# Kernel optimization log

Hardware: AMD Instinct MI355X
Metric: run time of the kernel (lower is better)

The kernel has to match this reference:

```python
import jax, jax.numpy as jnp
import numpy as np

DIM = 192
HEADS = 4
EPS = 1e-12  # matches torch F.normalize eps


def setup_inputs() -> dict:
    key = jax.random.key(0)
    ks = jax.random.split(key, 5)
    x = jax.random.normal(ks[0], (8, DIM, 128, 128), dtype=jnp.float32)
    # 1x1 conv_in: (3*dim, dim)
    w_in = jax.random.normal(ks[1], (3 * DIM, DIM), dtype=jnp.float32) * (1.0 / np.sqrt(DIM))
    # depthwise 3x3: OIHW with I=1, groups=3*dim -> (3*dim, 1, 3, 3)
    w_dw = jax.random.normal(ks[2], (3 * DIM, 1, 3, 3), dtype=jnp.float32) * (1.0 / 3.0)
    temperature = jnp.ones((HEADS, 1, 1), dtype=jnp.float32)
    # 1x1 conv_out: (dim, dim)
    w_out = jax.random.normal(ks[3], (DIM, DIM), dtype=jnp.float32) * (1.0 / np.sqrt(DIM))
    return {"x": x, "w_in": w_in, "w_dw": w_dw, "temperature": temperature, "w_out": w_out}


def _l2norm(t):
    n = jnp.sqrt(jnp.sum(t * t, axis=-1, keepdims=True))
    return t / jnp.maximum(n, EPS)


def reference(x, w_in, w_dw, temperature, w_out):
    b, c, h, w = x.shape
    # 1x1 pointwise conv (no bias)
    qkv = jnp.einsum('oc,bchw->bohw', w_in, x)
    # 3x3 depthwise conv, padding=1
    qkv = jax.lax.conv_general_dilated(
        qkv, w_dw, window_strides=(1, 1), padding=((1, 1), (1, 1)),
        feature_group_count=3 * c,
        dimension_numbers=('NCHW', 'OIHW', 'NCHW'))
    q, k, v = jnp.split(qkv, 3, axis=1)
    cph = c // HEADS  # channels per head
    hw = h * w
    q = q.reshape(b, HEADS, cph, hw)
    k = k.reshape(b, HEADS, cph, hw)
    v = v.reshape(b, HEADS, cph, hw)
    q = _l2norm(q)
    k = _l2norm(k)
    # channel-wise attention: [b, head, cph, cph]
    attn = jnp.einsum('bhcn,bhdn->bhcd', q, k) * temperature
    attn = jax.nn.softmax(attn, axis=-1)
    out = jnp.einsum('bhcd,bhdn->bhcn', attn, v)
    out = out.reshape(b, c, h, w)
    out = jnp.einsum('oc,bchw->bohw', w_out, out)
    return out
```

## Files before the change

### kernel.cpp

```cpp
#include <hip/hip_runtime.h>
#include <hip/hip_bf16.h>

#define HW 16384
#define NB 8
#define NC 192
#define NC3 576
#define NHEADS 4
#define CPH 48

typedef __attribute__((ext_vector_type(8))) short short8v;
typedef __attribute__((ext_vector_type(4))) float f32x4;

__device__ __forceinline__ float bf2f(ushort u) {
    union { unsigned int u; float f; } w; w.u = ((unsigned int)u) << 16; return w.f;
}
__device__ __forceinline__ ushort f2bf(float f) {
    union { float f; unsigned int u; } w; w.f = f;
    return (ushort)((w.u + 0x7FFFu + ((w.u >> 16) & 1u)) >> 16);
}

__global__ __launch_bounds__(256) void k_prep(const float* __restrict__ w_in,
                                              ushort* __restrict__ w_bf) {
    int i = blockIdx.x * 256 + threadIdx.x;
    if (i < NC3 * NC) w_bf[i] = f2bf(w_in[i]);
}

template<bool B_F32, bool OUT_F32>
__global__ __launch_bounds__(256) void k_gemm2(
    const ushort* __restrict__ Abase, long aStride, int MT,
    const void* __restrict__ Bp, long bStride,
    void* __restrict__ Op, long oStride)
{
    __shared__ ushort Bs[64 * 200];
    const int t = threadIdx.x;
    const int nt = blockIdx.x, b = blockIdx.y;

    {
        const int n0 = (t & 15) * 4;
        const int k0 = (t >> 4) * 12;
        ushort vals[12][4];
        if constexpr (B_F32) {
            const float* B = (const float*)Bp + (long)b * bStride
                           + (long)k0 * HW + nt * 64 + n0;
            #pragma unroll
            for (int kk = 0; kk < 12; kk++) {
                float4 v = *(const float4*)(B + (long)kk * HW);
                vals[kk][0] = f2bf(v.x); vals[kk][1] = f2bf(v.y);
                vals[kk][2] = f2bf(v.z); vals[kk][3] = f2bf(v.w);
            }
        } else {
            const ushort* B = (const ushort*)Bp + (long)b * bStride
                            + (long)k0 * HW + nt * 64 + n0;
            #pragma unroll
            for (int kk = 0; kk < 12; kk++) {
                ushort4 v = *(const ushort4*)(B + (long)kk * HW);
                vals[kk][0] = v.x; vals[kk][1] = v.y;
                vals[kk][2] = v.z; vals[kk][3] = v.w;
            }
        }
        #pragma unroll
        for (int i = 0; i < 4; i++) {
            #pragma unroll
            for (int seg = 0; seg < 3; seg++) {
                ushort4 w4;
                w4.x = vals[seg * 4 + 0][i];
                w4.y = vals[seg * 4 + 1][i];
                w4.z = vals[seg * 4 + 2][i];
                w4.w = vals[seg * 4 + 3][i];
                *(ushort4*)&Bs[(n0 + i) * 200 + k0 + seg * 4] = w4;
            }
        }
    }
    __syncthreads();

    const int wid = t >> 6, lane = t & 63;
    const int wm = (wid >> 1) * 32, wn = (wid & 1) * 32;
    const int lr = lane & 15, lk = lane >> 4;
    const ushort* Ab = Abase + (long)b * aStride;
    const ushort* Bs0 = &Bs[(wn + lr) * 200 + lk * 8];
    const f32x4 z4 = {0.f, 0.f, 0.f, 0.f};

    for (int ot = 0; ot < MT; ot++) {
        f32x4 acc[2][2];
        acc[0][0] = z4; acc[0][1] = z4; acc[1][0] = z4; acc[1][1] = z4;
        const ushort* Ar0 = Ab + (long)(ot * 64 + wm + lr) * NC + lk * 8;
        const ushort* Ar1 = Ar0 + 16 * NC;
        #pragma unroll
        for (int ks = 0; ks < 6; ks++) {
            short8v a0 = *(const short8v*)(Ar0 + ks * 32);
            short8v a1 = *(const short8v*)(Ar1 + ks * 32);
            short8v b0 = *(const short8v*)(Bs0 + ks * 32);
            short8v b1 = *(const short8v*)(Bs0 + 16 * 200 + ks * 32);
            acc[0][0] = __builtin_amdgcn_mfma_f32_16x16x32_bf16(a0, b0, acc[0][0], 0, 0, 0);
            acc[0][1] = __builtin_amdgcn_mfma_f32_16x16x32_bf16(a0, b1, acc[0][1], 0, 0, 0);
            acc[1][0] = __builtin_amdgcn_mfma_f32_16x16x32_bf16(a1, b0, acc[1][0], 0, 0, 0);
            acc[1][1] = __builtin_amdgcn_mfma_f32_16x16x32_bf16(a1, b1, acc[1][1], 0, 0, 0);
        }
        #pragma unroll
        for (int mi = 0; mi < 2; mi++) {
            #pragma unroll
            for (int ni = 0; ni < 2; ni++) {
                long gm = (long)ot * 64 + wm + mi * 16 + lk * 4;
                long gn = (long)nt * 64 + wn + ni * 16 + lr;
                if constexpr (OUT_F32) {
                    float* O = (float*)Op + (long)b * oStride + gm * HW + gn;
                    #pragma unroll
                    for (int r = 0; r < 4; r++) O[(long)r * HW] = acc[mi][ni][r];
                } else {
                    ushort* O = (ushort*)Op + (long)b * oStride + gm * HW + gn;
                    #pragma unroll
                    for (int r = 0; r < 4; r++) O[(long)r * HW] = f2bf(acc[mi][ni][r]);
                }
            }
        }
    }
}

__global__ __launch_bounds__(256) void k_dwconv(
    const ushort* __restrict__ qkv, const float* __restrict__ w_dw,
    ushort* __restrict__ qkv_dw, float* __restrict__ sumsq)
{
    __shared__ ushort tile[130 * 144];
    __shared__ float red[4];
    const int t = threadIdx.x;
    const int c = blockIdx.x, b = blockIdx.y;

    if (t < 144) { tile[t] = 0; tile[129 * 144 + t] = 0; }
    if (t < 128) { tile[(t + 1) * 144 + 7] = 0; tile[(t + 1) * 144 + 136] = 0; }

    const ushort* src = qkv + ((long)b * NC3 + c) * HW;
    #pragma unroll
    for (int i = 0; i < 8; i++) {
        int idx = t + 256 * i;
        int row = idx >> 4;
        int col8 = idx & 15;
        *(short8v*)(tile + (row + 1) * 144 + 8 + col8 * 8) =
            *(const short8v*)(src + (long)idx * 8);
    }
    __syncthreads();

    float wv[9];
    #pragma unroll
    for (int j = 0; j < 9; j++) wv[j] = w_dw[c * 9 + j];

    const int cb = (t & 15) * 8;
    const int r0 = (t >> 4) * 8;
    float win[3][16];

    auto load_row = [&](int tr, int slot) {
        #pragma unroll
        for (int j = 0; j < 4; j++) {
            ushort4 v = *(const ushort4*)(tile + tr * 144 + 4 + cb + j * 4);
            win[slot][j * 4 + 0] = bf2f(v.x);
            win[slot][j * 4 + 1] = bf2f(v.y);
            win[slot][j * 4 + 2] = bf2f(v.z);
            win[slot][j * 4 + 3] = bf2f(v.w);
        }
    };

    load_row(r0, 0);
    load_row(r0 + 1, 1);
    float ssq = 0.f;
    ushort* dst = qkv_dw + ((long)b * NC3 + c) * HW + (long)r0 * 128 + cb;

    #pragma unroll
    for (int rr = 0; rr < 8; rr++) {
        load_row(r0 + rr + 2, (rr + 2) % 3);
        const int s0 = rr % 3, s1 = (rr + 1) % 3, s2 = (rr + 2) % 3;
        short8v o;
        #pragma unroll
        for (int oc = 0; oc < 8; oc++) {
            float a = win[s0][oc + 3] * wv[0] + win[s0][oc + 4] * wv[1] + win[s0][oc + 5] * wv[2]
                    + win[s1][oc + 3] * wv[3] + win[s1][oc + 4] * wv[4] + win[s1][oc + 5] * wv[5]
                    + win[s2][oc + 3] * wv[6] + win[s2][oc + 4] * wv[7] + win[s2][oc + 5] * wv[8];
            ssq += a * a;
            o[oc] = (short)f2bf(a);
        }
        *(short8v*)(dst + rr * 128) = o;
    }

    #pragma unroll
    for (int off = 32; off > 0; off >>= 1) ssq += __shfl_down(ssq, off, 64);
    if ((t & 63) == 0) red[t >> 6] = ssq;
    __syncthreads();
    if (t == 0 && c < 2 * NC) sumsq[b * (2 * NC) + c] = red[0] + red[1] + red[2] + red[3];
}

__global__ __launch_bounds__(256) void k_scores(
    const ushort* __restrict__ qkv_dw, float* __restrict__ Spart)
{
    const int bh = blockIdx.x, ks = blockIdx.y;
    const int b = bh >> 2, h = bh & 3;
    const int t = threadIdx.x, wid = t >> 6, lane = t & 63;
    const int lr = lane & 15, lk = lane >> 4;
    const ushort* qb = qkv_dw + ((long)b * NC3 + h * CPH) * HW;
    const ushort* kb = qb + (long)NC * HW;

    const f32x4 z4 = {0.f, 0.f, 0.f, 0.f};
    f32x4 acc[3][3];
    #pragma unroll
    for (int i = 0; i < 3; i++) {
        #pragma unroll
        for (int j = 0; j < 3; j++) acc[i][j] = z4;
    }

    const int kstart = ks * 2048 + wid * 512;
    for (int k0 = kstart; k0 < kstart + 512; k0 += 32) {
        short8v a[3], bv[3];
        #pragma unroll
        for (int i = 0; i < 3; i++) {
            a[i]  = *(const short8v*)(qb + (long)(i * 16 + lr) * HW + k0 + lk * 8);
            bv[i] = *(const short8v*)(kb + (long)(i * 16 + lr) * HW + k0 + lk * 8);
        }
        #pragma unroll
        for (int mi = 0; mi < 3; mi++) {
            #pragma unroll
            for (int ni = 0; ni < 3; ni++)
                acc[mi][ni] = __builtin_amdgcn_mfma_f32_16x16x32_bf16(a[mi], bv[ni], acc[mi][ni], 0, 0, 0);
        }
    }

    __shared__ float Sb[4 * 48 * 48];
    #pragma unroll
    for (int mi = 0; mi < 3; mi++) {
        #pragma unroll
        for (int ni = 0; ni < 3; ni++) {
            #pragma unroll
            for (int r = 0; r < 4; r++)
                Sb[wid * 2304 + (mi * 16 + lk * 4 + r) * 48 + ni * 16 + lr] = acc[mi][ni][r];
        }
    }
    __syncthreads();
    float* outp = Spart + ((long)ks * 32 + bh) * 2304;
    for (int i = t; i < 2304; i += 256)
        outp[i] = Sb[i] + Sb[2304 + i] + Sb[4608 + i] + Sb[6912 + i];
}

__global__ __launch_bounds__(256) void k_final(
    const float* __restrict__ Spart, const float* __restrict__ sumsq,
    const float* __restrict__ temperature, const float* __restrict__ wout,
    ushort* __restrict__ Mmat)
{
    const int bh = blockIdx.x, b = bh >> 2, h = bh & 3;
    const int t = threadIdx.x;
    __shared__ float S[48 * 48];
    __shared__ float P[48 * 48];
    __shared__ float invq[48], invk[48];
    if (t < 48) {
        invq[t] = 1.f / fmaxf(sqrtf(sumsq[b * (2 * NC) + h * CPH + t]), 1e-12f);
        invk[t] = 1.f / fmaxf(sqrtf(sumsq[b * (2 * NC) + NC + h * CPH + t]), 1e-12f);
    }
    __syncthreads();
    const float T = temperature[h];
    for (int i = t; i < 2304; i += 256) {
        float s = 0.f;
        #pragma unroll
        for (int p = 0; p < 8; p++) s += Spart[((long)p * 32 + bh) * 2304 + i];
        int cc = i / 48, dd = i - cc * 48;
        S[i] = s * invq[cc] * invk[dd] * T;
    }
    __syncthreads();
    if (t < 48) {
        float m = -1e30f;
        for (int d = 0; d < 48; d++) m = fmaxf(m, S[t * 48 + d]);
        float sum = 0.f;
        for (int d = 0; d < 48; d++) { float e = __expf(S[t * 48 + d] - m); P[t * 48 + d] = e; sum += e; }
        float inv = 1.f / sum;
        for (int d = 0; d < 48; d++) P[t * 48 + d] *= inv;
    }
    __syncthreads();
    for (int i = t; i < NC * CPH; i += 256) {
        int o = i / 48, d = i - (i / 48) * 48;
        float a = 0.f;
        for (int c2 = 0; c2 < 48; c2++)
            a += wout[o * NC + h * CPH + c2] * P[c2 * 48 + d];
        Mmat[(long)b * NC * NC + (long)o * NC + h * CPH + d] = f2bf(a);
    }
}

extern "C" void kernel_launch(void* const* d_in, const int* in_sizes, int n_in,
                              void* d_out, int out_size, void* d_ws, size_t ws_size,
                              hipStream_t stream)
{
    (void)in_sizes; (void)n_in; (void)out_size;
    const float* x     = (const float*)d_in[0];
    const float* w_in  = (const float*)d_in[1];
    const float* w_dw  = (const float*)d_in[2];
    const float* temp  = (const float*)d_in[3];
    const float* w_out = (const float*)d_in[4];
    float* outp = (float*)d_out;

    const long QKV_BYTES = (long)NB * NC3 * HW * 2;
    char* ws = (char*)d_ws;
    if (ws_size < 305172480UL) return;
    ushort* qkv    = (ushort*)(ws);
    ushort* qkv_dw = (ushort*)(ws + QKV_BYTES);
    ushort* w_bf   = (ushort*)(ws + 2 * QKV_BYTES);
    float*  sumsq  = (float*) (ws + 302211072L);
    float*  Spart  = (float*) (ws + 302223360L);
    ushort* Mmat   = (ushort*)(ws + 304582656L);

    k_prep<<<dim3(432), 256, 0, stream>>>(w_in, w_bf);

    k_gemm2<true, false><<<dim3(256, NB), 256, 0, stream>>>(
        w_bf, 0L, 9, x, (long)NC * HW, qkv, (long)NC3 * HW);

    k_dwconv<<<dim3(NC3, NB), 256, 0, stream>>>(qkv, w_dw, qkv_dw, sumsq);

    k_scores<<<dim3(32, 8), 256, 0, stream>>>(qkv_dw, Spart);

    k_final<<<dim3(32), 256, 0, stream>>>(Spart, sumsq, temp, w_out, Mmat);

    k_gemm2<false, true><<<dim3(256, NB), 256, 0, stream>>>(
        Mmat, (long)NC * NC, 3, qkv_dw + (long)(2 * NC) * HW, (long)NC3 * HW,
        outp, (long)NC * HW);
}
```

Baseline: 301.1 us.

## Restructure pointwise GEMMs: register-resident A tile, pipelined B staging, vectorized stores

The 1x1-conv GEMM kernel changes its decomposition. Each block now keeps one 64-row weight tile in registers and walks over several 64-column spatial chunks, loading the next B chunk from global memory while the current one is converted and computed. The MFMA operands are swapped so each lane holds four consecutive spatial outputs, which allows float4/ushort4 stores in place of strided scalar ones. The LDS row pitch also changes from 200 to 208. The trade-off is that each block re-reads the x/v columns once per output-row tile instead of reusing them across all rows, and register pressure goes up.

```diff
diff --git a/kernel.cpp b/kernel.cpp
--- a/kernel.cpp
+++ b/kernel.cpp
@@ -25,94 +25,121 @@
     if (i < NC3 * NC) w_bf[i] = f2bf(w_in[i]);
 }
 
-template<bool B_F32, bool OUT_F32>
-__global__ __launch_bounds__(256) void k_gemm2(
-    const ushort* __restrict__ Abase, long aStride, int MT,
+template<bool B_F32, bool OUT_F32, int STEPS>
+__global__ __launch_bounds__(256) void k_gemm3(
+    const ushort* __restrict__ Abase, long aStride,
     const void* __restrict__ Bp, long bStride,
     void* __restrict__ Op, long oStride)
 {
-    __shared__ ushort Bs[64 * 200];
+    __shared__ ushort Bs[64][208];
     const int t = threadIdx.x;
-    const int nt = blockIdx.x, b = blockIdx.y;
-
-    {
-        const int n0 = (t & 15) * 4;
-        const int k0 = (t >> 4) * 12;
-        ushort vals[12][4];
-        if constexpr (B_F32) {
-            const float* B = (const float*)Bp + (long)b * bStride
-                           + (long)k0 * HW + nt * 64 + n0;
-            #pragma unroll
-            for (int kk = 0; kk < 12; kk++) {
-                float4 v = *(const float4*)(B + (long)kk * HW);
-                vals[kk][0] = f2bf(v.x); vals[kk][1] = f2bf(v.y);
-                vals[kk][2] = f2bf(v.z); vals[kk][3] = f2bf(v.w);
-            }
-        } else {
-            const ushort* B = (const ushort*)Bp + (long)b * bStride
-                            + (long)k0 * HW + nt * 64 + n0;
-            #pragma unroll
-            for (int kk = 0; kk < 12; kk++) {
-                ushort4 v = *(const ushort4*)(B + (long)kk * HW);
-                vals[kk][0] = v.x; vals[kk][1] = v.y;
-                vals[kk][2] = v.z; vals[kk][3] = v.w;
-            }
-        }
-        #pragma unroll
-        for (int i = 0; i < 4; i++) {
-            #pragma unroll
-            for (int seg = 0; seg < 3; seg++) {
-                ushort4 w4;
-                w4.x = vals[seg * 4 + 0][i];
-                w4.y = vals[seg * 4 + 1][i];
-                w4.z = vals[seg * 4 + 2][i];
-                w4.w = vals[seg * 4 + 3][i];
-                *(ushort4*)&Bs[(n0 + i) * 200 + k0 + seg * 4] = w4;
-            }
-        }
-    }
-    __syncthreads();
-
+    const int mt = blockIdx.x, ncnk = blockIdx.y, b = blockIdx.z;
     const int wid = t >> 6, lane = t & 63;
     const int wm = (wid >> 1) * 32, wn = (wid & 1) * 32;
     const int lr = lane & 15, lk = lane >> 4;
-    const ushort* Ab = Abase + (long)b * aStride;
-    const ushort* Bs0 = &Bs[(wn + lr) * 200 + lk * 8];
-    const f32x4 z4 = {0.f, 0.f, 0.f, 0.f};
-
-    for (int ot = 0; ot < MT; ot++) {
+
+    short8v a[2][6];
+    {
+        const ushort* A = Abase + (long)b * aStride
+                        + (long)(mt * 64 + wm + lr) * NC + lk * 8;
+        #pragma unroll
+        for (int mi = 0; mi < 2; mi++) {
+            #pragma unroll
+            for (int ks = 0; ks < 6; ks++)
+                a[mi][ks] = *(const short8v*)(A + mi * 16 * NC + ks * 32);
+        }
+    }
+
+    const int nl = (t & 15) * 4;
+    const int k0 = (t >> 4) * 12;
+    const long nbase = (long)ncnk * (STEPS * 64);
+
+    float4 fr[12];
+    ushort4 ur[12];
+
+    auto load_stage = [&](int s) {
+        long n0 = nbase + s * 64;
+        if constexpr (B_F32) {
+            const float* B = (const float*)Bp + (long)b * bStride
+                           + (long)k0 * HW + n0 + nl;
+            #pragma unroll
+            for (int kk = 0; kk < 12; kk++)
+                fr[kk] = *(const float4*)(B + (long)kk * HW);
+        } else {
+            const ushort* B = (const ushort*)Bp + (long)b * bStride
+                            + (long)k0 * HW + n0 + nl;
+            #pragma unroll
+            for (int kk = 0; kk < 12; kk++)
+                ur[kk] = *(const ushort4*)(B + (long)kk * HW);
+        }
+    };
+
+    auto write_stage = [&]() {
+        #pragma unroll
+        for (int i = 0; i < 4; i++) {
+            ushort e[12];
+            if constexpr (B_F32) {
+                #pragma unroll
+                for (int p = 0; p < 12; p++)
+                    e[p] = f2bf(((const float*)&fr[p])[i]);
+            } else {
+                #pragma unroll
+                for (int p = 0; p < 12; p++)
+                    e[p] = ((const ushort*)&ur[p])[i];
+            }
+            ushort* dst = &Bs[nl + i][k0];
+            #pragma unroll
+            for (int seg = 0; seg < 3; seg++) {
+                ushort4 w4;
+                w4.x = e[seg * 4 + 0]; w4.y = e[seg * 4 + 1];
+                w4.z = e[seg * 4 + 2]; w4.w = e[seg * 4 + 3];
+                *(ushort4*)(dst + seg * 4) = w4;
+            }
+        }
+    };
+
+    load_stage(0);
+    for (int s = 0; s < STEPS; s++) {
+        write_stage();
+        if (s + 1 < STEPS) load_stage(s + 1);
+        __syncthreads();
+
+        const f32x4 z4 = {0.f, 0.f, 0.f, 0.f};
         f32x4 acc[2][2];
         acc[0][0] = z4; acc[0][1] = z4; acc[1][0] = z4; acc[1][1] = z4;
-        const ushort* Ar0 = Ab + (long)(ot * 64 + wm + lr) * NC + lk * 8;
-        const ushort* Ar1 = Ar0 + 16 * NC;
+        const ushort* brow = &Bs[wn + lr][lk * 8];
         #pragma unroll
         for (int ks = 0; ks < 6; ks++) {
-            short8v a0 = *(const short8v*)(Ar0 + ks * 32);
-            short8v a1 = *(const short8v*)(Ar1 + ks * 32);
-            short8v b0 = *(const short8v*)(Bs0 + ks * 32);
-            short8v b1 = *(const short8v*)(Bs0 + 16 * 200 + ks * 32);
-            acc[0][0] = __builtin_amdgcn_mfma_f32_16x16x32_bf16(a0, b0, acc[0][0], 0, 0, 0);
-            acc[0][1] = __builtin_amdgcn_mfma_f32_16x16x32_bf16(a0, b1, acc[0][1], 0, 0, 0);
-            acc[1][0] = __builtin_amdgcn_mfma_f32_16x16x32_bf16(a1, b0, acc[1][0], 0, 0, 0);
-            acc[1][1] = __builtin_amdgcn_mfma_f32_16x16x32_bf16(a1, b1, acc[1][1], 0, 0, 0);
-        }
-        #pragma unroll
-        for (int mi = 0; mi < 2; mi++) {
-            #pragma unroll
-            for (int ni = 0; ni < 2; ni++) {
-                long gm = (long)ot * 64 + wm + mi * 16 + lk * 4;
-                long gn = (long)nt * 64 + wn + ni * 16 + lr;
+            short8v b0 = *(const short8v*)(brow + ks * 32);
+            short8v b1 = *(const short8v*)(brow + 16 * 208 + ks * 32);
+            acc[0][0] = __builtin_amdgcn_mfma_f32_16x16x32_bf16(b0, a[0][ks], acc[0][0], 0, 0, 0);
+            acc[0][1] = __builtin_amdgcn_mfma_f32_16x16x32_bf16(b0, a[1][ks], acc[0][1], 0, 0, 0);
+            acc[1][0] = __builtin_amdgcn_mfma_f32_16x16x32_bf16(b1, a[0][ks], acc[1][0], 0, 0, 0);
+            acc[1][1] = __builtin_amdgcn_mfma_f32_16x16x32_bf16(b1, a[1][ks], acc[1][1], 0, 0, 0);
+        }
+
+        long n0 = nbase + s * 64;
+        #pragma unroll
+        for (int ni = 0; ni < 2; ni++) {
+            #pragma unroll
+            for (int mi = 0; mi < 2; mi++) {
+                long m  = (long)(mt * 64 + wm + mi * 16 + lr);
+                long nn = n0 + wn + ni * 16 + lk * 4;
                 if constexpr (OUT_F32) {
-                    float* O = (float*)Op + (long)b * oStride + gm * HW + gn;
-                    #pragma unroll
-                    for (int r = 0; r < 4; r++) O[(long)r * HW] = acc[mi][ni][r];
+                    float* O = (float*)Op + (long)b * oStride + m * HW + nn;
+                    float4 v4 = make_float4(acc[ni][mi][0], acc[ni][mi][1],
+                                            acc[ni][mi][2], acc[ni][mi][3]);
+                    *(float4*)O = v4;
                 } else {
-                    ushort* O = (ushort*)Op + (long)b * oStride + gm * HW + gn;
-                    #pragma unroll
-                    for (int r = 0; r < 4; r++) O[(long)r * HW] = f2bf(acc[mi][ni][r]);
+                    ushort* O = (ushort*)Op + (long)b * oStride + m * HW + nn;
+                    ushort4 pk;
+                    pk.x = f2bf(acc[ni][mi][0]); pk.y = f2bf(acc[ni][mi][1]);
+                    pk.z = f2bf(acc[ni][mi][2]); pk.w = f2bf(acc[ni][mi][3]);
+                    *(ushort4*)O = pk;
                 }
             }
         }
+        __syncthreads();
     }
 }
 
@@ -302,8 +329,8 @@
 
     k_prep<<<dim3(432), 256, 0, stream>>>(w_in, w_bf);
 
-    k_gemm2<true, false><<<dim3(256, NB), 256, 0, stream>>>(
-        w_bf, 0L, 9, x, (long)NC * HW, qkv, (long)NC3 * HW);
+    k_gemm3<true, false, 8><<<dim3(9, 32, NB), 256, 0, stream>>>(
+        w_bf, 0L, x, (long)NC * HW, qkv, (long)NC3 * HW);
 
     k_dwconv<<<dim3(NC3, NB), 256, 0, stream>>>(qkv, w_dw, qkv_dw, sumsq);
 
@@ -311,7 +338,7 @@
 
     k_final<<<dim3(32), 256, 0, stream>>>(Spart, sumsq, temp, w_out, Mmat);
 
-    k_gemm2<false, true><<<dim3(256, NB), 256, 0, stream>>>(
-        Mmat, (long)NC * NC, 3, qkv_dw + (long)(2 * NC) * HW, (long)NC3 * HW,
+    k_gemm3<false, true, 4><<<dim3(3, 64, NB), 256, 0, stream>>>(
+        Mmat, (long)NC * NC, qkv_dw + (long)(2 * NC) * HW, (long)NC3 * HW,
         outp, (long)NC * HW);
 }
```

Result: slower. 317.6 us (+5.5%).
